# Kernel optimization log

Hardware: AMD Instinct MI355X
Metric: run time of the kernel (lower is better)

## Reference

```python
import jax, jax.numpy as jnp
import numpy as np

D_MODEL, D_FF, N_EXPERTS, TOP_K = 1024, 4096, 8, 2


def setup_inputs() -> dict:
    key = jax.random.key(0)
    ks = jax.random.split(key, 7)
    s = 0.02
    return {
        "x": jax.random.normal(ks[0], (2, 2048, D_MODEL), dtype=jnp.float32),
        "router_w": jax.random.normal(ks[1], (D_MODEL, N_EXPERTS), dtype=jnp.float32) * s,
        "router_b": jnp.zeros((N_EXPERTS,), dtype=jnp.float32),
        "w1": jax.random.normal(ks[2], (N_EXPERTS, D_MODEL, D_FF), dtype=jnp.float32) * s,
        "b1": jnp.zeros((N_EXPERTS, D_FF), dtype=jnp.float32),
        "w2": jax.random.normal(ks[3], (N_EXPERTS, D_FF, D_MODEL), dtype=jnp.float32) * s,
        "b2": jnp.zeros((N_EXPERTS, D_MODEL), dtype=jnp.float32),
    }


def reference(x, router_w, router_b, w1, b1, w2, b2):
    bsz, seq_len, d_model = x.shape
    flat_x = x.reshape(-1, d_model)                      # [T, D]
    logits = flat_x @ router_w + router_b                # [T, E]
    topk_scores, topk_idx = jax.lax.top_k(logits, TOP_K) # [T, K]
    gates = jax.nn.softmax(topk_scores, axis=-1).astype(flat_x.dtype)
    mixed = jnp.zeros_like(flat_x)
    num_experts = w1.shape[0]
    for e in range(num_experts):
        # dense per-expert MLP over all tokens; tokens not routed to e get weight 0,
        # so the math matches the original gather-MLP-scatter exactly.
        h = jax.nn.gelu(flat_x @ w1[e] + b1[e], approximate=False)  # exact GELU as torch nn.GELU
        y = h @ w2[e] + b2[e]                                       # [T, D]
        w_e = jnp.sum(jnp.where(topk_idx == e, gates, 0.0), axis=-1, keepdims=True)  # [T, 1]
        mixed = mixed + w_e * y
    return mixed.reshape(bsz, seq_len, d_model)
```

## Files before the change

### kernel.cpp

```cpp
#include <hip/hip_runtime.h>
#include <hip/hip_bf16.h>
#include <stdint.h>

#define T_TOK 4096
#define DM 1024
#define DF 4096
#define NE 8
#define PADROWS 9216

typedef __attribute__((ext_vector_type(8))) short short8;
typedef __attribute__((ext_vector_type(8))) unsigned short ushort8_t;
typedef __attribute__((ext_vector_type(4))) float f32x4;

__device__ __forceinline__ unsigned short f2bf(float f) {
    union { float f; unsigned u; } v; v.f = f;
    unsigned r = v.u + 0x7fffu + ((v.u >> 16) & 1u);
    return (unsigned short)(r >> 16);
}

__device__ __forceinline__ void async_cp16(const void* g, void* l) {
    __builtin_amdgcn_global_load_lds(
        (const __attribute__((address_space(1))) unsigned*)g,
        (__attribute__((address_space(3))) unsigned*)l,
        16, 0, 0);
}

__global__ __launch_bounds__(256) void k_router(
    const float* __restrict__ x, const float* __restrict__ rw,
    const float* __restrict__ rb, int* __restrict__ counts,
    int* __restrict__ listTok, float* __restrict__ listGate)
{
    int l  = threadIdx.x & 63;
    int wv = threadIdx.x >> 6;
    int t  = blockIdx.x * 4 + wv;
    const float* xr = x + (size_t)t * DM;
    float acc[NE];
#pragma unroll
    for (int e = 0; e < NE; ++e) acc[e] = 0.f;
#pragma unroll
    for (int i = 0; i < 16; ++i) {
        int d = i * 64 + l;
        float xv = xr[d];
        const float4* wp = (const float4*)(rw + (size_t)d * NE);
        float4 w0 = wp[0], w1 = wp[1];
        acc[0] += xv * w0.x; acc[1] += xv * w0.y; acc[2] += xv * w0.z; acc[3] += xv * w0.w;
        acc[4] += xv * w1.x; acc[5] += xv * w1.y; acc[6] += xv * w1.z; acc[7] += xv * w1.w;
    }
#pragma unroll
    for (int off = 32; off >= 1; off >>= 1)
#pragma unroll
        for (int e = 0; e < NE; ++e) acc[e] += __shfl_down(acc[e], off);
    if (l == 0) {
        float lg[NE];
#pragma unroll
        for (int e = 0; e < NE; ++e) lg[e] = acc[e] + rb[e];
        int i1 = 0; float s1 = lg[0];
#pragma unroll
        for (int e = 1; e < NE; ++e) if (lg[e] > s1) { s1 = lg[e]; i1 = e; }
        int i2 = -1; float s2 = -3.0e38f;
#pragma unroll
        for (int e = 0; e < NE; ++e) if (e != i1 && lg[e] > s2) { s2 = lg[e]; i2 = e; }
        float g1 = 1.f / (1.f + expf(s2 - s1));
        float g2 = 1.f - g1;
        int p1 = atomicAdd(&counts[i1], 1);
        listTok[i1 * T_TOK + p1] = t; listGate[i1 * T_TOK + p1] = g1;
        int p2 = atomicAdd(&counts[i2], 1);
        listTok[i2 * T_TOK + p2] = t; listGate[i2 * T_TOK + p2] = g2;
    }
}

__global__ void k_offsets(const int* __restrict__ counts, int* __restrict__ offsets)
{
    int cum = 0;
    for (int e = 0; e < NE; ++e) { offsets[e] = cum; cum += (counts[e] + 127) & ~127; }
    offsets[NE] = cum;
}

__global__ __launch_bounds__(256) void k_packw(const float* __restrict__ src,
                                               unsigned short* __restrict__ dst,
                                               int K, int N)
{
    __shared__ float tile[64][65];
    int e  = blockIdx.z;
    int n0 = blockIdx.x * 64;
    int k0 = blockIdx.y * 64;
    const float* s    = src + (size_t)e * K * N;
    unsigned short* d = dst + (size_t)e * K * N;
    int tid = threadIdx.x;
#pragma unroll
    for (int i = 0; i < 4; ++i) {
        int u  = i * 256 + tid;
        int kk = u >> 4;
        int nn = (u & 15) * 4;
        float4 v = *(const float4*)(s + (size_t)(k0 + kk) * N + n0 + nn);
        tile[kk][nn] = v.x; tile[kk][nn + 1] = v.y; tile[kk][nn + 2] = v.z; tile[kk][nn + 3] = v.w;
    }
    __syncthreads();
#pragma unroll
    for (int i = 0; i < 4; ++i) {
        int u  = i * 256 + tid;
        int nn = u >> 4;
        int g  = (u >> 1) & 7;
        int h  = (u & 1) * 4;
        int kc = g * 8 + h;
        int n  = n0 + nn;
        ushort4 o;
        o.x = f2bf(tile[kc + 0][nn]); o.y = f2bf(tile[kc + 1][nn]);
        o.z = f2bf(tile[kc + 2][nn]); o.w = f2bf(tile[kc + 3][nn]);
        int gp = g ^ (n & 7);
        size_t off = ((size_t)(k0 >> 6) * N + n) * 64 + gp * 8 + h;
        *(ushort4*)(d + off) = o;
    }
}

__global__ __launch_bounds__(256) void k_packa(
    const float* __restrict__ x, const int* __restrict__ listTok,
    const int* __restrict__ counts, const int* __restrict__ offsets,
    unsigned short* __restrict__ ap)
{
    int r0  = blockIdx.x * 64;
    int kt  = blockIdx.y;
    int tid = threadIdx.x;
    __shared__ int toks[64];
    if (tid < 64) {
        int r = r0 + tid;
        int tok = 0;
        int total = offsets[NE];
        if (r < total) {
            int e = 0;
#pragma unroll
            for (int j = 1; j < NE; ++j) if (r >= offsets[j]) e = j;
            int local = r - offsets[e];
            int c = counts[e];
            if (local >= c) local = c - 1;
            if (local < 0) local = 0;
            tok = listTok[e * T_TOK + local];
        }
        toks[tid] = tok;
    }
    __syncthreads();
#pragma unroll
    for (int i = 0; i < 4; ++i) {
        int u  = i * 256 + tid;
        int rl = u >> 4;
        int g  = (u >> 1) & 7;
        int h  = (u & 1) * 4;
        int tok = toks[rl];
        float4 v = *(const float4*)(x + (size_t)tok * DM + kt * 64 + g * 8 + h);
        ushort4 o; o.x = f2bf(v.x); o.y = f2bf(v.y); o.z = f2bf(v.z); o.w = f2bf(v.w);
        int row = r0 + rl;
        int gp  = g ^ (row & 7);
        size_t off = ((size_t)kt * PADROWS + row) * 64 + gp * 8 + h;
        *(ushort4*)(ap + off) = o;
    }
}

__global__ __launch_bounds__(256) void k_ffn1(
    const unsigned short* __restrict__ ap, const unsigned short* __restrict__ w1p,
    const float* __restrict__ b1, const int* __restrict__ counts,
    const int* __restrict__ offsets, unsigned short* __restrict__ Hp)
{
    __shared__ __align__(16) unsigned short lsA[128 * 64];
    __shared__ __align__(16) unsigned short lsB[128 * 64];
    int i  = blockIdx.x;
    int l0 = ((i & 7) << 10) + (i >> 3);
    int xx = l0 & 255, y = l0 >> 8;
    int e = xx >> 5, mt = xx & 31;
    int cnt = counts[e];
    int m0  = mt << 7;
    if (m0 >= cnt) return;
    int hbase = offsets[e];
    int n0    = y << 7;
    int tid = threadIdx.x, wv = tid >> 6, l = tid & 63;
    int wm = wv & 1, wn = wv >> 1;

    const unsigned short* srcA = ap + ((size_t)hbase + m0) * 64;
    const unsigned short* srcB = w1p + (size_t)e * DM * DF;

    f32x4 acc[4][4];
#pragma unroll
    for (int a = 0; a < 4; ++a)
#pragma unroll
        for (int b = 0; b < 4; ++b) acc[a][b] = (f32x4)(0.f);

    for (int kt = 0; kt < 16; ++kt) {
        const unsigned short* gA = srcA + (size_t)kt * PADROWS * 64;
        const unsigned short* gB = srcB + ((size_t)kt * DF + n0) * 64;
#pragma unroll
        for (int j = 0; j < 4; ++j) {
            int c = (wv * 4 + j) * 512;
            async_cp16(gA + c + l * 8, lsA + c);
            async_cp16(gB + c + l * 8, lsB + c);
        }
        __syncthreads();
#pragma unroll
        for (int ks = 0; ks < 2; ++ks) {
            short8 aF[4], bF[4];
#pragma unroll
            for (int mi = 0; mi < 4; ++mi) {
                int row = wm * 64 + mi * 16 + (l & 15);
                int g   = ks * 4 + (l >> 4);
                aF[mi] = *(const short8*)&lsA[row * 64 + ((g ^ (row & 7)) << 3)];
            }
#pragma unroll
            for (int ni = 0; ni < 4; ++ni) {
                int row = wn * 64 + ni * 16 + (l & 15);
                int g   = ks * 4 + (l >> 4);
                bF[ni] = *(const short8*)&lsB[row * 64 + ((g ^ (row & 7)) << 3)];
            }
#pragma unroll
            for (int mi = 0; mi < 4; ++mi)
#pragma unroll
                for (int ni = 0; ni < 4; ++ni)
                    acc[mi][ni] = __builtin_amdgcn_mfma_f32_16x16x32_bf16(aF[mi], bF[ni], acc[mi][ni], 0, 0, 0);
        }
        __syncthreads();
    }

    int q = l >> 4, cn = l & 15;
#pragma unroll
    for (int mi = 0; mi < 4; ++mi) {
#pragma unroll
        for (int ni = 0; ni < 4; ++ni) {
            int nloc = wn * 64 + ni * 16 + cn;
            float bias = b1[e * DF + n0 + nloc];
            unsigned short* base = (nloc & 64) ? lsB : lsA;
            int kc = nloc & 63, g = kc >> 3;
#pragma unroll
            for (int rg = 0; rg < 4; ++rg) {
                int m = wm * 64 + mi * 16 + q * 4 + rg;
                float v = acc[mi][ni][rg] + bias;
                v = 0.5f * v * (1.f + erff(v * 0.70710678118f));
                int gp = g ^ (m & 7);
                base[m * 64 + gp * 8 + (kc & 7)] = f2bf(v);
            }
        }
    }
    __syncthreads();
    {
        int c = tid >> 7;
        int r = tid & 127;
        const unsigned short* s = (c ? lsB : lsA) + r * 64;
        unsigned short* dst = Hp + (((size_t)(n0 >> 6) + c) * PADROWS + hbase + m0 + r) * 64;
#pragma unroll
        for (int j = 0; j < 8; ++j)
            *(ushort8_t*)(dst + j * 8) = *(const ushort8_t*)(s + j * 8);
    }
}

__global__ __launch_bounds__(256) void k_ffn2(
    const unsigned short* __restrict__ Hp, const unsigned short* __restrict__ w2p,
    const float* __restrict__ b2, const int* __restrict__ listTok,
    const float* __restrict__ listGate, const int* __restrict__ counts,
    const int* __restrict__ offsets, float* __restrict__ out)
{
    __shared__ __align__(16) unsigned short lsA[128 * 64];
    __shared__ __align__(16) unsigned short lsB[128 * 64];
    int i  = blockIdx.x;
    int l0 = ((i & 7) << 8) + (i >> 3);
    int xx = l0 & 255, y = l0 >> 8;
    int e = xx >> 5, mt = xx & 31;
    int cnt = counts[e];
    int m0  = mt << 7;
    if (m0 >= cnt) return;
    int hbase = offsets[e];
    int n0    = y << 7;
    int tid = threadIdx.x, wv = tid >> 6, l = tid & 63;
    int wm = wv & 1, wn = wv >> 1;

    const unsigned short* srcA = Hp + ((size_t)hbase + m0) * 64;
    const unsigned short* srcB = w2p + (size_t)e * DF * DM;

    f32x4 acc[4][4];
#pragma unroll
    for (int a = 0; a < 4; ++a)
#pragma unroll
        for (int b = 0; b < 4; ++b) acc[a][b] = (f32x4)(0.f);

    for (int kt = 0; kt < 64; ++kt) {
        const unsigned short* gA = srcA + (size_t)kt * PADROWS * 64;
        const unsigned short* gB = srcB + ((size_t)kt * DM + n0) * 64;
#pragma unroll
        for (int j = 0; j < 4; ++j) {
            int c = (wv * 4 + j) * 512;
            async_cp16(gA + c + l * 8, lsA + c);
            async_cp16(gB + c + l * 8, lsB + c);
        }
        __syncthreads();
#pragma unroll
        for (int ks = 0; ks < 2; ++ks) {
            short8 aF[4], bF[4];
#pragma unroll
            for (int mi = 0; mi < 4; ++mi) {
                int row = wm * 64 + mi * 16 + (l & 15);
                int g   = ks * 4 + (l >> 4);
                aF[mi] = *(const short8*)&lsA[row * 64 + ((g ^ (row & 7)) << 3)];
            }
#pragma unroll
            for (int ni = 0; ni < 4; ++ni) {
                int row = wn * 64 + ni * 16 + (l & 15);
                int g   = ks * 4 + (l >> 4);
                bF[ni] = *(const short8*)&lsB[row * 64 + ((g ^ (row & 7)) << 3)];
            }
#pragma unroll
            for (int mi = 0; mi < 4; ++mi)
#pragma unroll
                for (int ni = 0; ni < 4; ++ni)
                    acc[mi][ni] = __builtin_amdgcn_mfma_f32_16x16x32_bf16(aF[mi], bF[ni], acc[mi][ni], 0, 0, 0);
        }
        __syncthreads();
    }

    int q = l >> 4, cn = l & 15;
    const int*   lt  = listTok  + e * T_TOK;
    const float* lgt = listGate + e * T_TOK;
#pragma unroll
    for (int mi = 0; mi < 4; ++mi) {
#pragma unroll
        for (int rg = 0; rg < 4; ++rg) {
            int m = wm * 64 + mi * 16 + q * 4 + rg;
            int r = m0 + m;
            if (r < cnt) {
                int tok = lt[r];
                float ggt = lgt[r];
                float* orow = out + (size_t)tok * DM;
#pragma unroll
                for (int ni = 0; ni < 4; ++ni) {
                    int n = n0 + wn * 64 + ni * 16 + cn;
                    float v = acc[mi][ni][rg] + b2[e * DM + n];
                    atomicAdd(&orow[n], ggt * v);
                }
            }
        }
    }
}

extern "C" void kernel_launch(void* const* d_in, const int* in_sizes, int n_in,
                              void* d_out, int out_size, void* d_ws, size_t ws_size,
                              hipStream_t stream)
{
    const float* x  = (const float*)d_in[0];
    const float* rw = (const float*)d_in[1];
    const float* rb = (const float*)d_in[2];
    const float* w1 = (const float*)d_in[3];
    const float* b1 = (const float*)d_in[4];
    const float* w2 = (const float*)d_in[5];
    const float* b2 = (const float*)d_in[6];
    float* out = (float*)d_out;

    char* ws = (char*)d_ws;
    int*            counts   = (int*)(ws + 0);
    int*            offsets  = (int*)(ws + 128);
    int*            listTok  = (int*)(ws + 512);
    float*          listGate = (float*)(ws + 512 + 131072);
    unsigned short* apack    = (unsigned short*)(ws + 262656);
    unsigned short* w2p      = (unsigned short*)(ws + 262656);
    unsigned short* w1p      = (unsigned short*)(ws + 19137024);
    unsigned short* Hp       = (unsigned short*)(ws + 86245888);

    hipMemsetAsync(counts, 0, 32, stream);
    hipMemsetAsync(d_out, 0, (size_t)out_size * sizeof(float), stream);

    k_router <<<T_TOK / 4, 256, 0, stream>>>(x, rw, rb, counts, listTok, listGate);
    k_offsets<<<1, 1, 0, stream>>>(counts, offsets);
    k_packw  <<<dim3(DF / 64, DM / 64, NE), 256, 0, stream>>>(w1, w1p, DM, DF);
    k_packa  <<<dim3(PADROWS / 64, 16), 256, 0, stream>>>(x, listTok, counts, offsets, apack);
    k_ffn1   <<<NE * 32 * 32, 256, 0, stream>>>(apack, w1p, b1, counts, offsets, Hp);
    k_packw  <<<dim3(DM / 64, DF / 64, NE), 256, 0, stream>>>(w2, w2p, DF, DM);
    k_ffn2   <<<NE * 32 * 8, 256, 0, stream>>>(Hp, w2p, b2, listTok, listGate, counts, offsets, out);
}
```

Before: 697.4 us.

## Replace atomic scatter in FFN2 with per-row output buffer plus gather-combine kernel

FFN2 no longer atomically adds gated outputs into the output tensor. It writes biased rows to a padded per-expert staging buffer, and a new gather kernel combines each token's two expert rows with its gates. The router now records each token's expert and slot plus both gates. This removes fp32 atomics and the output memset, at the cost of an extra fp32 intermediate (about 40 MB) written and read back, plus one more launch. The block-index swizzle in both GEMMs changes to expert-interleaved ordering, and per-expert padding grows to 256 rows.

```diff
diff --git a/kernel.cpp b/kernel.cpp
--- a/kernel.cpp
+++ b/kernel.cpp
@@ -6,7 +6,7 @@
 #define DM 1024
 #define DF 4096
 #define NE 8
-#define PADROWS 9216
+#define PADROWS 10240
 
 typedef __attribute__((ext_vector_type(8))) short short8;
 typedef __attribute__((ext_vector_type(8))) unsigned short ushort8_t;
@@ -28,7 +28,8 @@
 __global__ __launch_bounds__(256) void k_router(
     const float* __restrict__ x, const float* __restrict__ rw,
     const float* __restrict__ rb, int* __restrict__ counts,
-    int* __restrict__ listTok, float* __restrict__ listGate)
+    int* __restrict__ listTok, int4* __restrict__ tokRec,
+    float2* __restrict__ tokGate)
 {
     int l  = threadIdx.x & 63;
     int wv = threadIdx.x >> 6;
@@ -63,16 +64,18 @@
         float g1 = 1.f / (1.f + expf(s2 - s1));
         float g2 = 1.f - g1;
         int p1 = atomicAdd(&counts[i1], 1);
-        listTok[i1 * T_TOK + p1] = t; listGate[i1 * T_TOK + p1] = g1;
+        listTok[i1 * T_TOK + p1] = t;
         int p2 = atomicAdd(&counts[i2], 1);
-        listTok[i2 * T_TOK + p2] = t; listGate[i2 * T_TOK + p2] = g2;
+        listTok[i2 * T_TOK + p2] = t;
+        tokRec[t]  = make_int4(i1, p1, i2, p2);
+        tokGate[t] = make_float2(g1, g2);
     }
 }
 
 __global__ void k_offsets(const int* __restrict__ counts, int* __restrict__ offsets)
 {
     int cum = 0;
-    for (int e = 0; e < NE; ++e) { offsets[e] = cum; cum += (counts[e] + 127) & ~127; }
+    for (int e = 0; e < NE; ++e) { offsets[e] = cum; cum += (counts[e] + 255) & ~255; }
     offsets[NE] = cum;
 }
 
@@ -134,7 +137,7 @@
             int c = counts[e];
             if (local >= c) local = c - 1;
             if (local < 0) local = 0;
-            tok = listTok[e * T_TOK + local];
+            tok = (c > 0) ? listTok[e * T_TOK + local] : 0;
         }
         toks[tid] = tok;
     }
@@ -163,9 +166,10 @@
     __shared__ __align__(16) unsigned short lsA[128 * 64];
     __shared__ __align__(16) unsigned short lsB[128 * 64];
     int i  = blockIdx.x;
-    int l0 = ((i & 7) << 10) + (i >> 3);
-    int xx = l0 & 255, y = l0 >> 8;
-    int e = xx >> 5, mt = xx & 31;
+    int e  = i & 7;
+    int j  = i >> 3;
+    int mt = j & 31;
+    int y  = j >> 5;
     int cnt = counts[e];
     int m0  = mt << 7;
     if (m0 >= cnt) return;
@@ -187,8 +191,8 @@
         const unsigned short* gA = srcA + (size_t)kt * PADROWS * 64;
         const unsigned short* gB = srcB + ((size_t)kt * DF + n0) * 64;
 #pragma unroll
-        for (int j = 0; j < 4; ++j) {
-            int c = (wv * 4 + j) * 512;
+        for (int jj = 0; jj < 4; ++jj) {
+            int c = (wv * 4 + jj) * 512;
             async_cp16(gA + c + l * 8, lsA + c);
             async_cp16(gB + c + l * 8, lsB + c);
         }
@@ -243,32 +247,32 @@
         const unsigned short* s = (c ? lsB : lsA) + r * 64;
         unsigned short* dst = Hp + (((size_t)(n0 >> 6) + c) * PADROWS + hbase + m0 + r) * 64;
 #pragma unroll
-        for (int j = 0; j < 8; ++j)
-            *(ushort8_t*)(dst + j * 8) = *(const ushort8_t*)(s + j * 8);
+        for (int jj = 0; jj < 8; ++jj)
+            *(ushort8_t*)(dst + jj * 8) = *(const ushort8_t*)(s + jj * 8);
     }
 }
 
 __global__ __launch_bounds__(256) void k_ffn2(
     const unsigned short* __restrict__ Hp, const unsigned short* __restrict__ w2p,
-    const float* __restrict__ b2, const int* __restrict__ listTok,
-    const float* __restrict__ listGate, const int* __restrict__ counts,
-    const int* __restrict__ offsets, float* __restrict__ out)
+    const float* __restrict__ b2, const int* __restrict__ counts,
+    const int* __restrict__ offsets, float* __restrict__ ypart)
 {
     __shared__ __align__(16) unsigned short lsA[128 * 64];
     __shared__ __align__(16) unsigned short lsB[128 * 64];
     int i  = blockIdx.x;
-    int l0 = ((i & 7) << 8) + (i >> 3);
-    int xx = l0 & 255, y = l0 >> 8;
-    int e = xx >> 5, mt = xx & 31;
+    int e  = i & 7;
+    int j  = i >> 3;
+    int mt = j & 31;
+    int y  = j >> 5;
     int cnt = counts[e];
     int m0  = mt << 7;
     if (m0 >= cnt) return;
-    int hbase = offsets[e];
-    int n0    = y << 7;
+    int R0 = offsets[e] + m0;
+    int n0 = y << 7;
     int tid = threadIdx.x, wv = tid >> 6, l = tid & 63;
     int wm = wv & 1, wn = wv >> 1;
 
-    const unsigned short* srcA = Hp + ((size_t)hbase + m0) * 64;
+    const unsigned short* srcA = Hp + (size_t)R0 * 64;
     const unsigned short* srcB = w2p + (size_t)e * DF * DM;
 
     f32x4 acc[4][4];
@@ -281,8 +285,8 @@
         const unsigned short* gA = srcA + (size_t)kt * PADROWS * 64;
         const unsigned short* gB = srcB + ((size_t)kt * DM + n0) * 64;
 #pragma unroll
-        for (int j = 0; j < 4; ++j) {
-            int c = (wv * 4 + j) * 512;
+        for (int jj = 0; jj < 4; ++jj) {
+            int c = (wv * 4 + jj) * 512;
             async_cp16(gA + c + l * 8, lsA + c);
             async_cp16(gB + c + l * 8, lsB + c);
         }
@@ -312,27 +316,41 @@
     }
 
     int q = l >> 4, cn = l & 15;
-    const int*   lt  = listTok  + e * T_TOK;
-    const float* lgt = listGate + e * T_TOK;
+    float bias[4];
+#pragma unroll
+    for (int ni = 0; ni < 4; ++ni) bias[ni] = b2[e * DM + n0 + wn * 64 + ni * 16 + cn];
 #pragma unroll
     for (int mi = 0; mi < 4; ++mi) {
 #pragma unroll
         for (int rg = 0; rg < 4; ++rg) {
             int m = wm * 64 + mi * 16 + q * 4 + rg;
-            int r = m0 + m;
-            if (r < cnt) {
-                int tok = lt[r];
-                float ggt = lgt[r];
-                float* orow = out + (size_t)tok * DM;
-#pragma unroll
-                for (int ni = 0; ni < 4; ++ni) {
-                    int n = n0 + wn * 64 + ni * 16 + cn;
-                    float v = acc[mi][ni][rg] + b2[e * DM + n];
-                    atomicAdd(&orow[n], ggt * v);
-                }
-            }
-        }
-    }
+            float* orow = ypart + ((size_t)R0 + m) * DM;
+#pragma unroll
+            for (int ni = 0; ni < 4; ++ni)
+                orow[n0 + wn * 64 + ni * 16 + cn] = acc[mi][ni][rg] + bias[ni];
+        }
+    }
+}
+
+__global__ __launch_bounds__(256) void k_gather(
+    const float* __restrict__ yp, const int4* __restrict__ rec,
+    const float2* __restrict__ gg, const int* __restrict__ offsets,
+    float* __restrict__ out)
+{
+    int t = blockIdx.x;
+    int4 rc = rec[t];
+    float2 w = gg[t];
+    size_t r1 = (size_t)offsets[rc.x] + rc.y;
+    size_t r2 = (size_t)offsets[rc.z] + rc.w;
+    const float4* a = (const float4*)(yp + r1 * DM);
+    const float4* b = (const float4*)(yp + r2 * DM);
+    float4 va = a[threadIdx.x], vb = b[threadIdx.x];
+    float4 o;
+    o.x = w.x * va.x + w.y * vb.x;
+    o.y = w.x * va.y + w.y * vb.y;
+    o.z = w.x * va.z + w.y * vb.z;
+    o.w = w.x * va.w + w.y * vb.w;
+    ((float4*)(out + (size_t)t * DM))[threadIdx.x] = o;
 }
 
 extern "C" void kernel_launch(void* const* d_in, const int* in_sizes, int n_in,
@@ -352,20 +370,22 @@
     int*            counts   = (int*)(ws + 0);
     int*            offsets  = (int*)(ws + 128);
     int*            listTok  = (int*)(ws + 512);
-    float*          listGate = (float*)(ws + 512 + 131072);
     unsigned short* apack    = (unsigned short*)(ws + 262656);
     unsigned short* w2p      = (unsigned short*)(ws + 262656);
-    unsigned short* w1p      = (unsigned short*)(ws + 19137024);
-    unsigned short* Hp       = (unsigned short*)(ws + 86245888);
+    unsigned short* w1p      = (unsigned short*)(ws + 21234176);
+    unsigned short* Hp       = (unsigned short*)(ws + 88343040);
+    float*          ypart    = (float*)(ws + 172229120);
+    int4*           tokRec   = (int4*)(ws + 214172160);
+    float2*         tokGate  = (float2*)(ws + 214237696);
 
     hipMemsetAsync(counts, 0, 32, stream);
-    hipMemsetAsync(d_out, 0, (size_t)out_size * sizeof(float), stream);
-
-    k_router <<<T_TOK / 4, 256, 0, stream>>>(x, rw, rb, counts, listTok, listGate);
+
+    k_router <<<T_TOK / 4, 256, 0, stream>>>(x, rw, rb, counts, listTok, tokRec, tokGate);
     k_offsets<<<1, 1, 0, stream>>>(counts, offsets);
     k_packw  <<<dim3(DF / 64, DM / 64, NE), 256, 0, stream>>>(w1, w1p, DM, DF);
     k_packa  <<<dim3(PADROWS / 64, 16), 256, 0, stream>>>(x, listTok, counts, offsets, apack);
     k_ffn1   <<<NE * 32 * 32, 256, 0, stream>>>(apack, w1p, b1, counts, offsets, Hp);
     k_packw  <<<dim3(DM / 64, DF / 64, NE), 256, 0, stream>>>(w2, w2p, DF, DM);
-    k_ffn2   <<<NE * 32 * 8, 256, 0, stream>>>(Hp, w2p, b2, listTok, listGate, counts, offsets, out);
-}
+    k_ffn2   <<<NE * 32 * 8, 256, 0, stream>>>(Hp, w2p, b2, counts, offsets, ypart);
+    k_gather <<<T_TOK, 256, 0, stream>>>(ypart, tokRec, tokGate, offsets, out);
+}
```

Result: faster. 652.7 us (-6.4%).
